# Kernel optimization log

Measured on AMD Instinct MI355X. Metric: run time of the kernel, lower is better.

The kernel has to match this reference:

```python
import jax, jax.numpy as jnp
import numpy as np

N_ITER = 15
ITER_LR = 0.1


def setup_inputs() -> dict:
    key = jax.random.key(0)
    ks = jax.random.split(key, 4)
    dims = [784, 512, 256, 10]
    x = jax.random.normal(ks[0], (32768, dims[0]), dtype=jnp.float32)
    # weights[i]: (dims[i+1], dims[i]) scaled by sqrt(2/dims[i+1]); biases[i]: (dims[i],) zeros
    W0 = jax.random.normal(ks[1], (dims[1], dims[0]), dtype=jnp.float32) * np.sqrt(2.0 / dims[1]).astype(np.float32)
    W1 = jax.random.normal(ks[2], (dims[2], dims[1]), dtype=jnp.float32) * np.sqrt(2.0 / dims[2]).astype(np.float32)
    W2 = jax.random.normal(ks[3], (dims[3], dims[2]), dtype=jnp.float32) * np.sqrt(2.0 / dims[3]).astype(np.float32)
    b0 = jnp.zeros((dims[0],), dtype=jnp.float32)
    b1 = jnp.zeros((dims[1],), dtype=jnp.float32)
    b2 = jnp.zeros((dims[2],), dtype=jnp.float32)
    return {"x": x, "W0": W0, "W1": W1, "W2": W2, "b0": b0, "b1": b1, "b2": b2}


def reference(x, W0, W1, W2, b0, b1, b2):
    # feedforward pass: mus[i+1] = relu(mus[i] @ W[i].T)
    m1 = jax.nn.relu(x @ W0.T)    # [B, 512]
    m2 = jax.nn.relu(m1 @ W1.T)   # [B, 256]
    m3 = jax.nn.relu(m2 @ W2.T)   # [B, 10]

    # iterative predictive-coding updates: for l in {1, 2}:
    #   pred = relu(mus[l+1] @ W[l] + b[l]); mus[l] = relu(mus[l] - iter_lr * (mus[l] - pred))
    def body(_, carry):
        m1, m2, m3 = carry
        pred1 = jax.nn.relu(m2 @ W1 + b1)                 # uses m2 before its update (loop order)
        m1 = jax.nn.relu(m1 - ITER_LR * (m1 - pred1))
        pred2 = jax.nn.relu(m3 @ W2 + b2)
        m2 = jax.nn.relu(m2 - ITER_LR * (m2 - pred2))
        return (m1, m2, m3)

    m1, m2, m3 = jax.lax.fori_loop(0, N_ITER, body, (m1, m2, m3))
    # mus[-1] is never updated by the loop; returned as-is (faithful to the torch code)
    return m3
```

## Files before the change

### kernel.cpp

```cpp
#include <hip/hip_runtime.h>

typedef __bf16 bhalf;
typedef bhalf bhalf8 __attribute__((ext_vector_type(8)));
typedef float f32x4 __attribute__((ext_vector_type(4)));
typedef unsigned short u16;
typedef u16 u16x8 __attribute__((ext_vector_type(8)));

__device__ __forceinline__ u16 f2bf(float f) {
  union { float f; unsigned u; } v; v.f = f;
  unsigned r = v.u + 0x7FFFu + ((v.u >> 16) & 1u);
  return (u16)(r >> 16);
}

__device__ __forceinline__ int swz(int L) { return L ^ (((L >> 7) & 7) << 4); }

#define GLL16(gp, lp) __builtin_amdgcn_global_load_lds( \
    (const __attribute__((address_space(1))) unsigned int*)(gp), \
    (__attribute__((address_space(3))) unsigned int*)(lp), 16, 0, 0)

#define KP0 800
#define W0E (512 * KP0)
#define W1E (256 * 512)
#define W2E (16 * 256)

__global__ __launch_bounds__(256) void cvt_weights(
    const float* __restrict__ W0, const float* __restrict__ W1,
    const float* __restrict__ W2,
    u16* __restrict__ W0b, u16* __restrict__ W1b, u16* __restrict__ W2b)
{
  int i = blockIdx.x * 256 + threadIdx.x;
  if (i < W0E) {
    int r = i / KP0, k = i - r * KP0;
    W0b[i] = (k < 784) ? f2bf(W0[r * 784 + k]) : (u16)0;
    return;
  }
  i -= W0E;
  if (i < W1E) { W1b[i] = f2bf(W1[i]); return; }
  i -= W1E;
  if (i < W2E) {
    int r = i >> 8, c = i & 255;
    W2b[i] = (r < 10) ? f2bf(W2[r * 256 + c]) : (u16)0;
  }
}

__global__ __launch_bounds__(512) void gemm1_fn(
    const float* __restrict__ x, const u16* __restrict__ Wb, u16* __restrict__ Cp)
{
  extern __shared__ u16 lds[];
  const int t = threadIdx.x, w = t >> 6, lane = t & 63;
  const size_t rbase = (size_t)blockIdx.x * 128;
  const int wr = w >> 2, wc = w & 3, fr = lane & 15, fg = lane >> 4;

  int aO[4], bO[8];
#pragma unroll
  for (int m = 0; m < 4; ++m) aO[m] = swz((wr * 64 + m * 16 + fr) * 64 + fg * 16);
#pragma unroll
  for (int n = 0; n < 8; ++n) bO[n] = swz((wc * 128 + n * 16 + fr) * 64 + fg * 16);

  const u16* bSrc[4];
#pragma unroll
  for (int i = 0; i < 4; ++i) {
    int P = (w * 4 + i) * 1024 + lane * 16;
    int U = swz(P);
    bSrc[i] = Wb + (size_t)(U >> 6) * KP0 + ((U & 63) >> 1);
  }

  const float* xRow; int aKe;
  {
    int P = t * 16;
    int U = swz(P);
    xRow = x + (rbase + (U >> 6)) * (size_t)784;
    aKe = (U & 63) >> 1;
  }

  f32x4 acc[4][8];
#pragma unroll
  for (int m = 0; m < 4; ++m)
#pragma unroll
    for (int n = 0; n < 8; ++n) acc[m][n] = (f32x4){0.f, 0.f, 0.f, 0.f};

  f32x4 xr0, xr1;
  bhalf8 bf[8], afA[4];

  auto loadX = [&](int s) {
    int gk = s * 32 + aKe;
    const float* p = xRow + ((gk < 784) ? gk : 0);
    xr0 = *(const f32x4*)p; xr1 = *(const f32x4*)(p + 4);
  };
  auto cvtW = [&](int aBase) {
    u16x8 v;
#pragma unroll
    for (int j = 0; j < 4; ++j) { v[j] = f2bf(xr0[j]); v[4 + j] = f2bf(xr1[j]); }
    *(u16x8*)((char*)lds + aBase + t * 16) = v;
  };
  auto stageB = [&](int s, int bBase) {
#pragma unroll
    for (int i = 0; i < 4; ++i)
      GLL16(bSrc[i] + s * 32, (char*)lds + bBase + (w * 4 + i) * 1024);
  };
  auto rdA = [&](int aB) {
#pragma unroll
    for (int m = 0; m < 4; ++m) afA[m] = *(const bhalf8*)((const char*)lds + aB + aO[m]);
  };
  auto rdB = [&](int bB) {
#pragma unroll
    for (int n = 0; n < 8; ++n) bf[n] = *(const bhalf8*)((const char*)lds + bB + bO[n]);
  };
  auto mfmaLo = [&]() {
    __builtin_amdgcn_s_setprio(1);
#pragma unroll
    for (int m = 0; m < 4; ++m)
#pragma unroll
      for (int n = 0; n < 4; ++n)
        acc[m][n] = __builtin_amdgcn_mfma_f32_16x16x32_bf16(afA[m], bf[n], acc[m][n], 0, 0, 0);
    __builtin_amdgcn_s_setprio(0);
  };
  auto mfmaHi = [&]() {
    __builtin_amdgcn_s_setprio(1);
#pragma unroll
    for (int m = 0; m < 4; ++m)
#pragma unroll
      for (int n = 4; n < 8; ++n)
        acc[m][n] = __builtin_amdgcn_mfma_f32_16x16x32_bf16(afA[m], bf[n], acc[m][n], 0, 0, 0);
    __builtin_amdgcn_s_setprio(0);
  };

  loadX(0);
  stageB(0, 16384);
  cvtW(0);
  loadX(1);
  stageB(1, 16384 + 32768);
  asm volatile("s_waitcnt vmcnt(6) lgkmcnt(0)" ::: "memory");
  __builtin_amdgcn_s_barrier();

  for (int tt = 0; tt < 23; ++tt) {
    const int c = tt & 1;
    const int aB = c * 8192;
    const int bB = 16384 + c * 32768;
    rdA(aB); rdB(bB);
    mfmaLo();
    asm volatile("s_waitcnt lgkmcnt(0)" ::: "memory");
    __builtin_amdgcn_s_barrier();
    cvtW(aB ^ 8192);
    loadX(tt + 2);
    stageB(tt + 2, bB);
    mfmaHi();
    asm volatile("s_waitcnt vmcnt(6) lgkmcnt(0)" ::: "memory");
    __builtin_amdgcn_s_barrier();
  }
  {
    rdA(8192); rdB(16384 + 32768);
    mfmaLo();
    asm volatile("s_waitcnt lgkmcnt(0)" ::: "memory");
    __builtin_amdgcn_s_barrier();
    cvtW(0);
    mfmaHi();
    asm volatile("s_waitcnt vmcnt(0) lgkmcnt(0)" ::: "memory");
    __builtin_amdgcn_s_barrier();

    rdA(0); rdB(16384);
    mfmaLo();
    mfmaHi();
  }

#pragma unroll
  for (int m = 0; m < 4; ++m)
#pragma unroll
    for (int n = 0; n < 8; ++n)
#pragma unroll
      for (int q = 0; q < 4; ++q) {
        size_t row = rbase + wr * 64 + m * 16 + fg * 4 + q;
        size_t col = (size_t)wc * 128 + n * 16 + fr;
        float vv = acc[m][n][q];
        vv = vv > 0.f ? vv : 0.f;
        Cp[row * 512 + col] = f2bf(vv);
      }
}

__global__ __launch_bounds__(512, 4) void gemm23(
    const u16* __restrict__ m1, const u16* __restrict__ W1b,
    const u16* __restrict__ W2b, float* __restrict__ out)
{
  __shared__ u16 pool[20480];
  __shared__ u16 W2s[16][264];
  const int t = threadIdx.x, w = t >> 6, lane = t & 63;
  const size_t rbase = (size_t)blockIdx.x * 64;
  const int wr = w >> 2, wc = w & 3, fr = lane & 15, fg = lane >> 4;

  {
    int r = t >> 5, kc = (t & 31) * 8;
    *(int4*)&W2s[r][kc] = *(const int4*)(W2b + r * 256 + kc);
  }

  int aOff[2], bOff[4];
#pragma unroll
  for (int i = 0; i < 2; ++i) aOff[i] = swz((wr * 32 + i * 16 + fr) * 64 + fg * 16);
#pragma unroll
  for (int j = 0; j < 4; ++j) bOff[j] = swz((wc * 64 + j * 16 + fr) * 64 + fg * 16);

  const u16* aSrc = nullptr; int aDst = 0;
  if (w < 4) {
    int Dl = (w * 64 + lane) * 16;
    int Ul = swz(Dl);
    aSrc = m1 + (rbase + (Ul >> 6)) * 512 + ((Ul & 63) >> 1);
    aDst = (w * 64) * 16;
  }
  const u16* bSrc[2]; int bDst[2];
#pragma unroll
  for (int i = 0; i < 2; ++i) {
    int Dl = (w * 128 + i * 64 + lane) * 16;
    int Ul = swz(Dl);
    bSrc[i] = W1b + (Ul >> 6) * 512 + ((Ul & 63) >> 1);
    bDst[i] = 8192 + (w * 128 + i * 64) * 16;
  }

  f32x4 acc[2][4];
#pragma unroll
  for (int i = 0; i < 2; ++i)
#pragma unroll
    for (int j = 0; j < 4; ++j) acc[i][j] = (f32x4){0.f, 0.f, 0.f, 0.f};

  if (w < 4) GLL16(aSrc, (char*)pool + aDst);
#pragma unroll
  for (int i = 0; i < 2; ++i) GLL16(bSrc[i], (char*)pool + bDst[i]);

  for (int tt = 0; tt < 16; ++tt) {
    const int cur = tt & 1;
    const char* Asc = (const char*)pool + cur * 4096;
    const char* Bsc = (const char*)pool + 8192 + cur * 16384;
    asm volatile("s_waitcnt vmcnt(0)" ::: "memory");
    __syncthreads();

    if (tt < 15) {
      const int k0 = (tt + 1) * 32;
      if (w < 4) GLL16(aSrc + k0, (char*)pool + (cur ^ 1) * 4096 + aDst);
#pragma unroll
      for (int i = 0; i < 2; ++i)
        GLL16(bSrc[i] + k0, (char*)pool + (cur ^ 1) * 16384 + bDst[i]);
    }

    bhalf8 af[2], bfv[4];
#pragma unroll
    for (int i = 0; i < 2; ++i) af[i] = *(const bhalf8*)(Asc + aOff[i]);
#pragma unroll
    for (int j = 0; j < 4; ++j) bfv[j] = *(const bhalf8*)(Bsc + bOff[j]);
#pragma unroll
    for (int i = 0; i < 2; ++i)
#pragma unroll
      for (int j = 0; j < 4; ++j)
        acc[i][j] = __builtin_amdgcn_mfma_f32_16x16x32_bf16(af[i], bfv[j], acc[i][j], 0, 0, 0);
  }

  __syncthreads();
#pragma unroll
  for (int i = 0; i < 2; ++i)
#pragma unroll
    for (int j = 0; j < 4; ++j)
#pragma unroll
      for (int q = 0; q < 4; ++q) {
        int row = wr * 32 + i * 16 + fg * 4 + q;
        int col = wc * 64 + j * 16 + fr;
        float vv = acc[i][j][q];
        vv = vv > 0.f ? vv : 0.f;
        pool[row * 264 + col] = f2bf(vv);
      }
  __syncthreads();

  if (w < 4) {
    f32x4 acc3 = (f32x4){0.f, 0.f, 0.f, 0.f};
    const int arow = w * 16 + fr;
#pragma unroll
    for (int ks = 0; ks < 8; ++ks) {
      bhalf8 a = *(const bhalf8*)&pool[arow * 264 + ks * 32 + fg * 8];
      bhalf8 b = *(const bhalf8*)&W2s[fr][ks * 32 + fg * 8];
      acc3 = __builtin_amdgcn_mfma_f32_16x16x32_bf16(a, b, acc3, 0, 0, 0);
    }
    if (fr < 10) {
#pragma unroll
      for (int q = 0; q < 4; ++q) {
        size_t row = rbase + w * 16 + fg * 4 + q;
        float vv = acc3[q];
        out[row * 10 + fr] = vv > 0.f ? vv : 0.f;
      }
    }
  }
}

extern "C" void kernel_launch(void* const* d_in, const int* in_sizes, int n_in,
                              void* d_out, int out_size, void* d_ws, size_t ws_size,
                              hipStream_t stream) {
  const float* x  = (const float*)d_in[0];
  const float* W0 = (const float*)d_in[1];
  const float* W1 = (const float*)d_in[2];
  const float* W2 = (const float*)d_in[3];
  float* out = (float*)d_out;

  char* ws = (char*)d_ws;
  u16* m1  = (u16*)(ws);
  u16* W0b = (u16*)(ws + 33554432);
  u16* W1b = (u16*)(ws + 34373632);
  u16* W2b = (u16*)(ws + 34635776);

  hipFuncSetAttribute((const void*)gemm1_fn,
                      hipFuncAttributeMaxDynamicSharedMemorySize, 81920);

  cvt_weights<<<dim3((W0E + W1E + W2E + 255) / 256), dim3(256), 0, stream>>>(
      W0, W1, W2, W0b, W1b, W2b);

  gemm1_fn<<<dim3(256), dim3(512), 81920, stream>>>(x, W0b, m1);

  gemm23<<<dim3(512), dim3(512), 0, stream>>>(m1, W1b, W2b, out);
}
```

Before: 65.64 us.

## Restructure gemm1 with K=64 A tiles and triple-buffered B staging

Reworks the first GEMM's main loop so each tile covers K=64 for A (converted x) and splits B into K=32 halves held in a three-deep LDS ring. The weight padding grows from 800 to 832 so the K dimension divides evenly, and the loop is fully unrolled into 13 tiles. MFMA work is split into quarter phases, each fenced by barriers, with explicit vmcnt waits and sched_barriers to control how loads and MFMAs interleave. The intent is deeper prefetch and fewer loop iterations, in exchange for 128KB of LDS per block, more barriers, and a larger padded weight buffer.

```diff
diff --git a/kernel.cpp b/kernel.cpp
--- a/kernel.cpp
+++ b/kernel.cpp
@@ -18,7 +18,9 @@
     (const __attribute__((address_space(1))) unsigned int*)(gp), \
     (__attribute__((address_space(3))) unsigned int*)(lp), 16, 0, 0)
 
-#define KP0 800
+#define SB() __builtin_amdgcn_sched_barrier(0)
+
+#define KP0 832
 #define W0E (512 * KP0)
 #define W1E (256 * 512)
 #define W2E (16 * 256)
@@ -43,34 +45,36 @@
   }
 }
 
-__global__ __launch_bounds__(512) void gemm1_fn(
+__global__ __launch_bounds__(512) void gemm1_p8(
     const float* __restrict__ x, const u16* __restrict__ Wb, u16* __restrict__ Cp)
 {
-  extern __shared__ u16 lds[];
+  extern __shared__ u16 ldsu[];
+  char* lds = (char*)ldsu;
   const int t = threadIdx.x, w = t >> 6, lane = t & 63;
   const size_t rbase = (size_t)blockIdx.x * 128;
   const int wr = w >> 2, wc = w & 3, fr = lane & 15, fg = lane >> 4;
 
-  int aO[4], bO[8];
-#pragma unroll
-  for (int m = 0; m < 4; ++m) aO[m] = swz((wr * 64 + m * 16 + fr) * 64 + fg * 16);
-#pragma unroll
-  for (int n = 0; n < 8; ++n) bO[n] = swz((wc * 128 + n * 16 + fr) * 64 + fg * 16);
-
-  const u16* bSrc[4];
+  int aO[4];
+#pragma unroll
+  for (int m = 0; m < 4; ++m) aO[m] = swz((wr * 64 + m * 16 + fr) * 128 + fg * 16);
+  int bO[4];
+#pragma unroll
+  for (int j = 0; j < 4; ++j) bO[j] = swz((wc * 128 + j * 16 + fr) * 64 + fg * 16);
+
+  const u16* bSrcP[4];
 #pragma unroll
   for (int i = 0; i < 4; ++i) {
     int P = (w * 4 + i) * 1024 + lane * 16;
     int U = swz(P);
-    bSrc[i] = Wb + (size_t)(U >> 6) * KP0 + ((U & 63) >> 1);
-  }
-
-  const float* xRow; int aKe;
-  {
-    int P = t * 16;
+    bSrcP[i] = Wb + (size_t)(U >> 6) * KP0 + ((U & 63) >> 1);
+  }
+  const float* xRow[2]; int aKc[2];
+#pragma unroll
+  for (int c2 = 0; c2 < 2; ++c2) {
+    int P = c2 * 8192 + t * 16;
     int U = swz(P);
-    xRow = x + (rbase + (U >> 6)) * (size_t)784;
-    aKe = (U & 63) >> 1;
+    xRow[c2] = x + (rbase + (U >> 7)) * (size_t)784;
+    aKc[c2] = (U & 127) >> 1;
   }
 
   f32x4 acc[4][8];
@@ -79,34 +83,47 @@
 #pragma unroll
     for (int n = 0; n < 8; ++n) acc[m][n] = (f32x4){0.f, 0.f, 0.f, 0.f};
 
-  f32x4 xr0, xr1;
-  bhalf8 bf[8], afA[4];
-
-  auto loadX = [&](int s) {
-    int gk = s * 32 + aKe;
-    const float* p = xRow + ((gk < 784) ? gk : 0);
-    xr0 = *(const f32x4*)p; xr1 = *(const f32x4*)(p + 4);
-  };
-  auto cvtW = [&](int aBase) {
-    u16x8 v;
-#pragma unroll
-    for (int j = 0; j < 4; ++j) { v[j] = f2bf(xr0[j]); v[4 + j] = f2bf(xr1[j]); }
-    *(u16x8*)((char*)lds + aBase + t * 16) = v;
-  };
-  auto stageB = [&](int s, int bBase) {
-#pragma unroll
-    for (int i = 0; i < 4; ++i)
-      GLL16(bSrc[i] + s * 32, (char*)lds + bBase + (w * 4 + i) * 1024);
-  };
-  auto rdA = [&](int aB) {
-#pragma unroll
-    for (int m = 0; m < 4; ++m) afA[m] = *(const bhalf8*)((const char*)lds + aB + aO[m]);
-  };
-  auto rdB = [&](int bB) {
-#pragma unroll
-    for (int n = 0; n < 8; ++n) bf[n] = *(const bhalf8*)((const char*)lds + bB + bO[n]);
-  };
-  auto mfmaLo = [&]() {
+  bhalf8 afA[4], bf[4];
+  f32x4 xrE[2][2], xrO[2][2];
+
+  auto loadX = [&](int tt2, f32x4 (&xr)[2][2]) {
+#pragma unroll
+    for (int c2 = 0; c2 < 2; ++c2) {
+      int k = tt2 * 64 + aKc[c2];
+      const float* p = xRow[c2] + ((k < 784) ? k : 0);
+      xr[c2][0] = *(const f32x4*)p; xr[c2][1] = *(const f32x4*)(p + 4);
+    }
+  };
+  auto cvtW = [&](int aB, f32x4 (&xr)[2][2]) {
+#pragma unroll
+    for (int c2 = 0; c2 < 2; ++c2) {
+      u16x8 v;
+#pragma unroll
+      for (int j = 0; j < 4; ++j) { v[j] = f2bf(xr[c2][0][j]); v[4 + j] = f2bf(xr[c2][1][j]); }
+      *(u16x8*)(lds + aB + c2 * 8192 + t * 16) = v;
+    }
+  };
+  auto gllLo = [&](int H) {
+    char* bb = lds + 32768 + (H % 3) * 32768;
+    GLL16(bSrcP[0] + H * 32, bb + (w * 4 + 0) * 1024);
+    GLL16(bSrcP[1] + H * 32, bb + (w * 4 + 1) * 1024);
+  };
+  auto gllHi = [&](int H) {
+    char* bb = lds + 32768 + (H % 3) * 32768;
+    GLL16(bSrcP[2] + H * 32, bb + (w * 4 + 2) * 1024);
+    GLL16(bSrcP[3] + H * 32, bb + (w * 4 + 3) * 1024);
+  };
+  auto rdA = [&](int aB, int ks) {
+#pragma unroll
+    for (int m = 0; m < 4; ++m)
+      afA[m] = *(const bhalf8*)(lds + aB + (aO[m] ^ (ks << 6)));
+  };
+  auto rdBq = [&](int H, int hi) {
+    const char* bb = lds + 32768 + (H % 3) * 32768 + hi * 4096;
+#pragma unroll
+    for (int j = 0; j < 4; ++j) bf[j] = *(const bhalf8*)(bb + bO[j]);
+  };
+  auto mfmaLoQ = [&]() {
     __builtin_amdgcn_s_setprio(1);
 #pragma unroll
     for (int m = 0; m < 4; ++m)
@@ -115,53 +132,67 @@
         acc[m][n] = __builtin_amdgcn_mfma_f32_16x16x32_bf16(afA[m], bf[n], acc[m][n], 0, 0, 0);
     __builtin_amdgcn_s_setprio(0);
   };
-  auto mfmaHi = [&]() {
+  auto mfmaHiQ = [&]() {
     __builtin_amdgcn_s_setprio(1);
 #pragma unroll
     for (int m = 0; m < 4; ++m)
 #pragma unroll
-      for (int n = 4; n < 8; ++n)
-        acc[m][n] = __builtin_amdgcn_mfma_f32_16x16x32_bf16(afA[m], bf[n], acc[m][n], 0, 0, 0);
+      for (int n = 0; n < 4; ++n)
+        acc[m][4 + n] = __builtin_amdgcn_mfma_f32_16x16x32_bf16(afA[m], bf[n], acc[m][4 + n], 0, 0, 0);
     __builtin_amdgcn_s_setprio(0);
   };
 
-  loadX(0);
-  stageB(0, 16384);
-  cvtW(0);
-  loadX(1);
-  stageB(1, 16384 + 32768);
-  asm volatile("s_waitcnt vmcnt(6) lgkmcnt(0)" ::: "memory");
+  auto tile = [&](int tt, f32x4 (&xrLd)[2][2], f32x4 (&xrCv)[2][2],
+                  bool doStage, bool doX, int vmPh4, bool vm0Ph2) {
+    const int aB = (tt & 1) * 16384;
+    const int H0 = 2 * tt, H1 = 2 * tt + 1;
+    rdA(aB, 0); rdBq(H0, 0);
+    if (doStage) gllLo(H0 + 2);
+    __builtin_amdgcn_s_barrier();
+    asm volatile("s_waitcnt lgkmcnt(0)" ::: "memory"); SB();
+    mfmaLoQ();
+    __builtin_amdgcn_s_barrier();
+    rdBq(H0, 1);
+    if (doStage) gllHi(H0 + 2);
+    __builtin_amdgcn_s_barrier();
+    asm volatile("s_waitcnt lgkmcnt(0)" ::: "memory"); SB();
+    mfmaHiQ();
+    if (vm0Ph2) { asm volatile("s_waitcnt vmcnt(0)" ::: "memory"); }
+    else        { asm volatile("s_waitcnt vmcnt(4)" ::: "memory"); }
+    __builtin_amdgcn_s_barrier();
+    rdA(aB, 1); rdBq(H1, 0);
+    if (doStage) gllLo(H1 + 2);
+    if (doX) loadX(tt + 2, xrLd);
+    __builtin_amdgcn_s_barrier();
+    asm volatile("s_waitcnt lgkmcnt(0)" ::: "memory"); SB();
+    mfmaLoQ();
+    __builtin_amdgcn_s_barrier();
+    rdBq(H1, 1);
+    if (tt < 12) cvtW(aB ^ 16384, xrCv);
+    if (doStage) gllHi(H1 + 2);
+    __builtin_amdgcn_s_barrier();
+    asm volatile("s_waitcnt lgkmcnt(0)" ::: "memory"); SB();
+    mfmaHiQ();
+    if (vmPh4 == 8)      { asm volatile("s_waitcnt vmcnt(8)" ::: "memory"); }
+    else if (vmPh4 == 4) { asm volatile("s_waitcnt vmcnt(4)" ::: "memory"); }
+    __builtin_amdgcn_s_barrier();
+  };
+
+  gllLo(0); gllHi(0);
+  gllLo(1); gllHi(1);
+  loadX(0, xrE);
+  loadX(1, xrO);
+  cvtW(0, xrE);
+  asm volatile("s_waitcnt lgkmcnt(0)" ::: "memory");
   __builtin_amdgcn_s_barrier();
 
-  for (int tt = 0; tt < 23; ++tt) {
-    const int c = tt & 1;
-    const int aB = c * 8192;
-    const int bB = 16384 + c * 32768;
-    rdA(aB); rdB(bB);
-    mfmaLo();
-    asm volatile("s_waitcnt lgkmcnt(0)" ::: "memory");
-    __builtin_amdgcn_s_barrier();
-    cvtW(aB ^ 8192);
-    loadX(tt + 2);
-    stageB(tt + 2, bB);
-    mfmaHi();
-    asm volatile("s_waitcnt vmcnt(6) lgkmcnt(0)" ::: "memory");
-    __builtin_amdgcn_s_barrier();
-  }
-  {
-    rdA(8192); rdB(16384 + 32768);
-    mfmaLo();
-    asm volatile("s_waitcnt lgkmcnt(0)" ::: "memory");
-    __builtin_amdgcn_s_barrier();
-    cvtW(0);
-    mfmaHi();
-    asm volatile("s_waitcnt vmcnt(0) lgkmcnt(0)" ::: "memory");
-    __builtin_amdgcn_s_barrier();
-
-    rdA(0); rdB(16384);
-    mfmaLo();
-    mfmaHi();
-  }
+  for (int i = 0; i < 5; ++i) {
+    tile(2 * i,     xrE, xrO, true, true, 8, false);
+    tile(2 * i + 1, xrO, xrE, true, true, 8, false);
+  }
+  tile(10, xrE, xrO, true,  true,  8, false);
+  tile(11, xrO, xrE, true,  false, 4, false);
+  tile(12, xrE, xrO, false, false, -1, true);
 
 #pragma unroll
   for (int m = 0; m < 4; ++m)
@@ -298,16 +329,16 @@
   char* ws = (char*)d_ws;
   u16* m1  = (u16*)(ws);
   u16* W0b = (u16*)(ws + 33554432);
-  u16* W1b = (u16*)(ws + 34373632);
-  u16* W2b = (u16*)(ws + 34635776);
-
-  hipFuncSetAttribute((const void*)gemm1_fn,
-                      hipFuncAttributeMaxDynamicSharedMemorySize, 81920);
+  u16* W1b = (u16*)(ws + 34406400);
+  u16* W2b = (u16*)(ws + 34668544);
+
+  hipFuncSetAttribute((const void*)gemm1_p8,
+                      hipFuncAttributeMaxDynamicSharedMemorySize, 131072);
 
   cvt_weights<<<dim3((W0E + W1E + W2E + 255) / 256), dim3(256), 0, stream>>>(
       W0, W1, W2, W0b, W1b, W2b);
 
-  gemm1_fn<<<dim3(256), dim3(512), 81920, stream>>>(x, W0b, m1);
+  gemm1_p8<<<dim3(256), dim3(512), 131072, stream>>>(x, W0b, m1);
 
   gemm23<<<dim3(512), dim3(512), 0, stream>>>(m1, W1b, W2b, out);
 }
```

After: 62.76 us. 4.4% less time.
